# Kernel optimization log

Hardware: AMD Instinct MI355X
Metric: run time of the kernel (lower is better)

The kernel has to match this reference:

```python
import jax, jax.numpy as jnp
import numpy as np

N_NODES = 10000
N_EDGES = 160000
N_REL = 4
N_GRAPHS = 256
IN_DIM = 64


def rgcn_layer(x, W, root, bias, src, dst, etype, num_nodes, num_rel):
    # PyG RGCNConv with default aggr='mean': per-relation mean aggregation,
    # plus root transform and bias.
    h = jnp.einsum('nd,rdf->rnf', x, W)            # [R, N, F] grouped GEMM
    msg = h[etype, src]                             # [E, F] gather per edge
    comb = dst * num_rel + etype                    # (dst, relation) bucket
    cnt = jax.ops.segment_sum(jnp.ones(etype.shape, x.dtype), comb,
                              num_segments=num_nodes * num_rel)
    inv = 1.0 / jnp.maximum(cnt, 1.0)
    msg = msg * inv[comb][:, None]                  # per-relation mean norm
    agg = jax.ops.segment_sum(msg, dst, num_segments=num_nodes)  # scatter-add
    return agg + x @ root + bias


def global_mean_pool(x, batch, num_graphs):
    s = jax.ops.segment_sum(x, batch, num_segments=num_graphs)
    c = jax.ops.segment_sum(jnp.ones(batch.shape, x.dtype), batch,
                            num_segments=num_graphs)
    return s / jnp.maximum(c, 1.0)[:, None]


def setup_inputs() -> dict:
    key = jax.random.key(0)
    ks = jax.random.split(key, 20)
    s = 0.02
    inp = {
        'x': jax.random.normal(ks[0], (N_NODES, IN_DIM), jnp.float32),
        'edge_index': jax.random.randint(ks[1], (2, N_EDGES), 0, N_NODES),
        'edge_type': jax.random.randint(ks[2], (N_EDGES,), 0, N_REL),
        'batch': jnp.sort(jax.random.randint(ks[3], (N_NODES,), 0, N_GRAPHS)),
        'W1': jax.random.normal(ks[4], (N_REL, IN_DIM, 1024), jnp.float32) * s,
        'root1': jax.random.normal(ks[5], (IN_DIM, 1024), jnp.float32) * s,
        'b1': jnp.zeros((1024,), jnp.float32),
        'W2': jax.random.normal(ks[6], (N_REL, 1024, 1024), jnp.float32) * s,
        'root2': jax.random.normal(ks[7], (1024, 1024), jnp.float32) * s,
        'b2': jnp.zeros((1024,), jnp.float32),
        'W3': jax.random.normal(ks[8], (N_REL, 1024, 712), jnp.float32) * s,
        'root3': jax.random.normal(ks[9], (1024, 712), jnp.float32) * s,
        'b3': jnp.zeros((712,), jnp.float32),
        'fw1': jax.random.normal(ks[10], (712, 64), jnp.float32) * s,
        'fb1': jnp.zeros((64,), jnp.float32),
        'fw2': jax.random.normal(ks[11], (64, 1), jnp.float32) * s,
        'fb2': jnp.zeros((1,), jnp.float32),
    }
    return inp


def reference(x, edge_index, edge_type, batch, W1, root1, b1, W2, root2, b2,
              W3, root3, b3, fw1, fb1, fw2, fb2):
    src, dst = edge_index[0], edge_index[1]
    # dropout is a no-op in eval mode (training=False)
    h = jax.nn.relu(rgcn_layer(x, W1, root1, b1, src, dst, edge_type, N_NODES, N_REL))
    h = jax.nn.relu(rgcn_layer(h, W2, root2, b2, src, dst, edge_type, N_NODES, N_REL))
    h = jax.nn.relu(rgcn_layer(h, W3, root3, b3, src, dst, edge_type, N_NODES, N_REL))
    g = global_mean_pool(h, batch, N_GRAPHS)        # [G, 712]
    g = jax.nn.relu(g @ fw1 + fb1)
    out = g @ fw2 + fb2                             # [G, 1]
    return out
```

## Files before the change

### kernel.cpp

```cpp
#include <hip/hip_runtime.h>
#include <stdint.h>

#define N_NODES 10000
#define N_EDGES 160000
#define N_REL   4
#define N_GRAPHS 256
#define NBUCKET (N_NODES * N_REL)

typedef __attribute__((ext_vector_type(8))) short short8;
typedef __attribute__((ext_vector_type(4))) float float4v;

__device__ __forceinline__ unsigned short f2bf(float f) {
  unsigned int u = __float_as_uint(f);
  u = u + 0x7FFFu + ((u >> 16) & 1u);
  return (unsigned short)(u >> 16);
}
__device__ __forceinline__ float bf2f(unsigned short b) {
  return __uint_as_float(((unsigned int)b) << 16);
}

__device__ __forceinline__ void g2lds16(const void* g, void* l) {
  __builtin_amdgcn_global_load_lds(
      (const __attribute__((address_space(1))) void*)g,
      (__attribute__((address_space(3))) void*)l, 16, 0, 0);
}

__device__ __forceinline__ int lower_bound_i(const int* a, int n, int key) {
  int lo = 0, hi = n;
  while (lo < hi) { int mid = (lo + hi) >> 1; if (a[mid] < key) lo = mid + 1; else hi = mid; }
  return lo;
}

__global__ void count_edges_k(const int* __restrict__ ei, const int* __restrict__ et,
                              int* __restrict__ cnt, int E) {
  int e = blockIdx.x * 256 + threadIdx.x;
  if (e < E) atomicAdd(&cnt[ei[E + e] * N_REL + et[e]], 1);
}

__global__ void scan_block_k(const int* __restrict__ cnt, int* __restrict__ eexcl,
                             int* __restrict__ btot, int n) {
  int i = blockIdx.x * 256 + threadIdx.x;
  int v = (i < n) ? cnt[i] : 0;
  int lane = threadIdx.x & 63, wv = threadIdx.x >> 6;
  int s = v;
  #pragma unroll
  for (int off = 1; off < 64; off <<= 1) {
    int t = __shfl_up(s, off, 64);
    if (lane >= off) s += t;
  }
  __shared__ int wt[4];
  if (lane == 63) wt[wv] = s;
  __syncthreads();
  int wadd = 0;
  for (int w = 0; w < wv; ++w) wadd += wt[w];
  int incl = s + wadd;
  if (i < n) eexcl[i] = incl - v;
  if (threadIdx.x == 255) btot[blockIdx.x] = incl;
}

__global__ void scan_final_k(const int* __restrict__ cnt, const int* __restrict__ eexcl,
                             const int* __restrict__ btot, int* __restrict__ offs,
                             int* __restrict__ cursor, float* __restrict__ inv, int n) {
  __shared__ int wred[4];
  __shared__ int sboff;
  int t = threadIdx.x;
  int part = (t < (int)blockIdx.x) ? btot[t] : 0;
  #pragma unroll
  for (int off = 32; off > 0; off >>= 1) part += __shfl_down(part, off, 64);
  if ((t & 63) == 0) wred[t >> 6] = part;
  __syncthreads();
  if (t == 0) sboff = wred[0] + wred[1] + wred[2] + wred[3];
  __syncthreads();
  int i = blockIdx.x * 256 + t;
  if (i < n) {
    int o = sboff + eexcl[i];
    offs[i] = o;
    cursor[i] = o;
    int c = cnt[i];
    inv[i] = 1.0f / (float)(c > 1 ? c : 1);
  }
}

__global__ void fill_csr_k(const int* __restrict__ ei, const int* __restrict__ et,
                           int* __restrict__ cursor, int* __restrict__ elist, int E) {
  int e = blockIdx.x * 256 + threadIdx.x;
  if (e >= E) return;
  int dst = ei[E + e], src = ei[e], r = et[e];
  int pos = atomicAdd(&cursor[dst * N_REL + r], 1);
  elist[pos] = src;
}

__global__ void wcat_transpose_k(const float* __restrict__ W, const float* __restrict__ root,
                                 unsigned short* __restrict__ out, int Din4, int F, int K) {
  __shared__ float tile[32][33];
  int kb = blockIdx.x * 32, fb = blockIdx.y * 32;
  for (int i = threadIdx.y; i < 32; i += 8) {
    int k = kb + i, f = fb + threadIdx.x;
    float v = 0.0f;
    if (k < K && f < F) v = (k < Din4) ? W[(size_t)k * F + f] : root[(size_t)(k - Din4) * F + f];
    tile[i][threadIdx.x] = v;
  }
  __syncthreads();
  for (int i = threadIdx.y; i < 32; i += 8) {
    int f = fb + i, k = kb + threadIdx.x;
    if (f < F && k < K) out[(size_t)f * K + k] = f2bf(tile[threadIdx.x][i]);
  }
}

__global__ void aggregate64_k(const float* __restrict__ x, const int* __restrict__ offs,
                              const int* __restrict__ cnt, const float* __restrict__ inv,
                              const int* __restrict__ elist, unsigned short* __restrict__ Xcat) {
  const int n = blockIdx.x;
  const int wv = threadIdx.x >> 6;
  const int col = threadIdx.x & 63;
  const int b = n * N_REL + wv;
  const int start = offs[b], c = cnt[b];
  const float sc = inv[b];
  float acc = 0.0f;
  for (int j = 0; j < c; ++j) {
    int s = elist[start + j];
    acc += x[(size_t)s * 64 + col];
  }
  Xcat[(size_t)n * 320 + wv * 64 + col] = f2bf(acc * sc);
  if (wv == 0)
    Xcat[(size_t)n * 320 + 256 + col] = f2bf(x[(size_t)n * 64 + col]);
}

__global__ __launch_bounds__(64) void aggregate_bf16_k(
    const unsigned short* __restrict__ h,
    const int* __restrict__ offs, const int* __restrict__ cnt,
    const float* __restrict__ inv, const int* __restrict__ elist,
    unsigned short* __restrict__ Xcat) {
  const int bid = blockIdx.x;
  const int chunk = bid & 7;
  const int n = bid >> 3;
  const int lane = threadIdx.x;
  const int col = chunk * 128 + lane * 2;
  const int Din = 1024, K5 = 5120;
  const int b0 = n * N_REL;
  #pragma unroll
  for (int r = 0; r < N_REL; ++r) {
    const int s0 = offs[b0 + r];
    const int c = cnt[b0 + r];
    const float sc = inv[b0 + r];
    float a0 = 0.f, a1 = 0.f;
    for (int j = 0; j < c; ++j) {
      int s = elist[s0 + j];
      ushort2 v = *(const ushort2*)(h + (size_t)s * Din + col);
      a0 += bf2f(v.x); a1 += bf2f(v.y);
    }
    ushort2 o;
    o.x = f2bf(a0 * sc); o.y = f2bf(a1 * sc);
    *(ushort2*)&Xcat[(size_t)n * K5 + r * Din + col] = o;
  }
  *(ushort2*)&Xcat[(size_t)n * K5 + 4 * Din + col] =
      *(const ushort2*)(h + (size_t)n * Din + col);
}

__global__ __launch_bounds__(256) void gemm_bt_bias_relu_k(
    const short* __restrict__ A, const short* __restrict__ Bt,
    const float* __restrict__ bias, unsigned short* __restrict__ C,
    int M, int Ndim, int K, int NX) {
  __shared__ short As[128 * 64];
  __shared__ short Bs[128 * 64];

  const int bid = blockIdx.x;
  const int xcd = bid & 7;
  const int local = bid >> 3;
  const int t = xcd * (NX * 10) + local;
  const int tileM = t / NX;
  const int tileN = t - tileM * NX;
  const int mBase = tileM * 128;
  const int nBase = tileN * 128;

  const int tid = threadIdx.x;
  const int wave = tid >> 6;
  const int lane = tid & 63;
  const int half = lane >> 4;
  const int lrow = lane & 15;
  const int wm = (wave >> 1) * 64;
  const int wn = (wave & 1) * 64;
  const int srow = lane >> 3;
  const int schunk = (lane & 7) ^ srow;

  float4v acc[4][4] = {};

  for (int k0 = 0; k0 < K; k0 += 64) {
    #pragma unroll
    for (int p = 0; p < 4; ++p) {
      int rb = wave * 32 + p * 8;
      int r = rb + srow;
      int gr = mBase + r; if (gr > M - 1) gr = M - 1;
      g2lds16(A + (size_t)gr * K + k0 + schunk * 8, &As[rb * 64]);
      int gn = nBase + r; if (gn > Ndim - 1) gn = Ndim - 1;
      g2lds16(Bt + (size_t)gn * K + k0 + schunk * 8, &Bs[rb * 64]);
    }
    __syncthreads();

    #pragma unroll
    for (int kk = 0; kk < 2; ++kk) {
      short8 a[4], b[4];
      #pragma unroll
      for (int i = 0; i < 4; ++i) {
        int r = wm + i * 16 + lrow;
        int q = (kk * 4 + half) ^ (r & 7);
        a[i] = *(const short8*)&As[r * 64 + q * 8];
      }
      #pragma unroll
      for (int j = 0; j < 4; ++j) {
        int r = wn + j * 16 + lrow;
        int q = (kk * 4 + half) ^ (r & 7);
        b[j] = *(const short8*)&Bs[r * 64 + q * 8];
      }
      #pragma unroll
      for (int i = 0; i < 4; ++i)
        #pragma unroll
        for (int j = 0; j < 4; ++j)
          acc[i][j] = __builtin_amdgcn_mfma_f32_16x16x32_bf16(a[i], b[j], acc[i][j], 0, 0, 0);
    }
    __syncthreads();
  }

  #pragma unroll
  for (int i = 0; i < 4; ++i) {
    int row0 = mBase + wm + i * 16 + half * 4;
    #pragma unroll
    for (int j = 0; j < 4; ++j) {
      int col = nBase + wn + j * 16 + lrow;
      if (col < Ndim) {
        float bv = bias[col];
        #pragma unroll
        for (int r = 0; r < 4; ++r) {
          int rr = row0 + r;
          if (rr < M) C[(size_t)rr * Ndim + col] = f2bf(fmaxf(acc[i][j][r] + bv, 0.0f));
        }
      }
    }
  }
}

__global__ __launch_bounds__(256) void pool_mlp_k(
    const unsigned short* __restrict__ h, const int* __restrict__ batch,
    const float* __restrict__ fw1, const float* __restrict__ fb1,
    const float* __restrict__ fw2, const float* __restrict__ fb2,
    float* __restrict__ out, int N, int F) {
  __shared__ float gsh[712];
  __shared__ float part[4][64];

  const int gid = blockIdx.x;
  const int tid = threadIdx.x;
  const int lo = lower_bound_i(batch, N, gid);
  const int hi = lower_bound_i(batch, N, gid + 1);
  const float scale = (hi > lo) ? 1.0f / (float)(hi - lo) : 0.0f;
  const int C4 = F >> 2;

  if (tid < C4) {
    float a0 = 0.f, a1 = 0.f, a2 = 0.f, a3 = 0.f;
    for (int n = lo; n < hi; ++n) {
      ushort4 v = *(const ushort4*)(h + (size_t)n * F + tid * 4);
      a0 += bf2f(v.x); a1 += bf2f(v.y); a2 += bf2f(v.z); a3 += bf2f(v.w);
    }
    gsh[tid * 4 + 0] = a0 * scale;
    gsh[tid * 4 + 1] = a1 * scale;
    gsh[tid * 4 + 2] = a2 * scale;
    gsh[tid * 4 + 3] = a3 * scale;
  }
  __syncthreads();

  const int f = tid & 63;
  const int wv = tid >> 6;
  const int d0 = wv * 178;
  const int d1 = min(d0 + 178, F);
  float a = 0.0f;
  int d = d0;
  for (; d + 3 < d1; d += 4) {
    float g0 = gsh[d], g1 = gsh[d + 1], g2 = gsh[d + 2], g3 = gsh[d + 3];
    a += g0 * fw1[(size_t)d * 64 + f]
       + g1 * fw1[(size_t)(d + 1) * 64 + f]
       + g2 * fw1[(size_t)(d + 2) * 64 + f]
       + g3 * fw1[(size_t)(d + 3) * 64 + f];
  }
  for (; d < d1; ++d) a += gsh[d] * fw1[(size_t)d * 64 + f];
  part[wv][f] = a;
  __syncthreads();

  if (tid < 64) {
    float hsum = part[0][tid] + part[1][tid] + part[2][tid] + part[3][tid] + fb1[tid];
    hsum = fmaxf(hsum, 0.0f);
    float p = hsum * fw2[tid];
    #pragma unroll
    for (int off = 32; off > 0; off >>= 1) p += __shfl_down(p, off, 64);
    if (tid == 0) out[gid] = p + fb2[0];
  }
}

extern "C" void kernel_launch(void* const* d_in, const int* in_sizes, int n_in,
                              void* d_out, int out_size, void* d_ws, size_t ws_size,
                              hipStream_t stream) {
  (void)in_sizes; (void)n_in; (void)out_size;
  const float* x    = (const float*)d_in[0];
  const int*  ei    = (const int*)d_in[1];
  const int*  et    = (const int*)d_in[2];
  const int*  batch = (const int*)d_in[3];
  const float* W1 = (const float*)d_in[4],  *root1 = (const float*)d_in[5],  *b1 = (const float*)d_in[6];
  const float* W2 = (const float*)d_in[7],  *root2 = (const float*)d_in[8],  *b2 = (const float*)d_in[9];
  const float* W3 = (const float*)d_in[10], *root3 = (const float*)d_in[11], *b3 = (const float*)d_in[12];
  const float* fw1 = (const float*)d_in[13], *fb1 = (const float*)d_in[14];
  const float* fw2 = (const float*)d_in[15], *fb2 = (const float*)d_in[16];
  float* out = (float*)d_out;

  char* ws = (char*)d_ws;
  size_t off = 0;
  auto alloc = [&](size_t bytes) -> void* {
    void* p = ws + off; off += (bytes + 255) & ~(size_t)255; return p;
  };
  int*   cnt    = (int*)alloc(NBUCKET * 4);
  int*   offs   = (int*)alloc(NBUCKET * 4);
  int*   cursor = (int*)alloc(NBUCKET * 4);
  int*   eexcl  = (int*)alloc(NBUCKET * 4);
  int*   btot   = (int*)alloc(256 * 4);
  int*   elist  = (int*)alloc(N_EDGES * 4);
  float* inv    = (float*)alloc(NBUCKET * 4);
  unsigned short* Xcat  = (unsigned short*)alloc((size_t)N_NODES * 5120 * 2);
  unsigned short* WcatT = (unsigned short*)alloc((size_t)1024 * 5120 * 2);
  unsigned short* hA = (unsigned short*)alloc((size_t)N_NODES * 1024 * 2);
  unsigned short* hB = (unsigned short*)alloc((size_t)N_NODES * 1024 * 2);
  (void)ws_size;

  hipMemsetAsync(cnt, 0, NBUCKET * 4, stream);
  count_edges_k<<<(N_EDGES + 255) / 256, 256, 0, stream>>>(ei, et, cnt, N_EDGES);
  int nsb = (NBUCKET + 255) / 256;
  scan_block_k<<<nsb, 256, 0, stream>>>(cnt, eexcl, btot, NBUCKET);
  scan_final_k<<<nsb, 256, 0, stream>>>(cnt, eexcl, btot, offs, cursor, inv, NBUCKET);
  fill_csr_k<<<(N_EDGES + 255) / 256, 256, 0, stream>>>(ei, et, cursor, elist, N_EDGES);

  wcat_transpose_k<<<dim3(10, 32), dim3(32, 8), 0, stream>>>(W1, root1, WcatT, 256, 1024, 320);
  aggregate64_k<<<N_NODES, 256, 0, stream>>>(x, offs, cnt, inv, elist, Xcat);
  gemm_bt_bias_relu_k<<<8 * 80, 256, 0, stream>>>(
      (const short*)Xcat, (const short*)WcatT, b1, hA, N_NODES, 1024, 320, 8);

  wcat_transpose_k<<<dim3(160, 32), dim3(32, 8), 0, stream>>>(W2, root2, WcatT, 4096, 1024, 5120);
  aggregate_bf16_k<<<N_NODES * 8, 64, 0, stream>>>(hA, offs, cnt, inv, elist, Xcat);
  gemm_bt_bias_relu_k<<<8 * 80, 256, 0, stream>>>(
      (const short*)Xcat, (const short*)WcatT, b2, hB, N_NODES, 1024, 5120, 8);

  wcat_transpose_k<<<dim3(160, 23), dim3(32, 8), 0, stream>>>(W3, root3, WcatT, 4096, 712, 5120);
  aggregate_bf16_k<<<N_NODES * 8, 64, 0, stream>>>(hB, offs, cnt, inv, elist, Xcat);
  gemm_bt_bias_relu_k<<<6 * 80, 256, 0, stream>>>(
      (const short*)Xcat, (const short*)WcatT, b3, hA, N_NODES, 712, 5120, 6);

  pool_mlp_k<<<N_GRAPHS, 256, 0, stream>>>(hA, batch, fw1, fb1, fw2, fb2, out,
                                           N_NODES, 712);
}
```

Baseline: 596.7 us.

## Parallelize relation buckets across waves and batch edge-index loads in aggregation

The bf16 aggregation kernel now uses 256-thread blocks, so each of four waves handles one relation bucket at the same time instead of looping over relations serially. Edge indices are loaded cooperatively, 64 at a time per wave, and broadcast with shuffles. The gather loop is unrolled by four to keep more independent loads in flight. Outputs are written with nontemporal stores to avoid polluting the cache, at the cost of idle waves when relation bucket sizes are uneven.

Result: slower. 667.9 us (+11.9%).

```diff
diff --git a/kernel.cpp b/kernel.cpp
--- a/kernel.cpp
+++ b/kernel.cpp
@@ -126,7 +126,7 @@
     Xcat[(size_t)n * 320 + 256 + col] = f2bf(x[(size_t)n * 64 + col]);
 }
 
-__global__ __launch_bounds__(64) void aggregate_bf16_k(
+__global__ __launch_bounds__(256) void aggregate_bf16_k(
     const unsigned short* __restrict__ h,
     const int* __restrict__ offs, const int* __restrict__ cnt,
     const float* __restrict__ inv, const int* __restrict__ elist,
@@ -134,27 +134,45 @@
   const int bid = blockIdx.x;
   const int chunk = bid & 7;
   const int n = bid >> 3;
-  const int lane = threadIdx.x;
+  const int wv = threadIdx.x >> 6;
+  const int lane = threadIdx.x & 63;
   const int col = chunk * 128 + lane * 2;
   const int Din = 1024, K5 = 5120;
-  const int b0 = n * N_REL;
-  #pragma unroll
-  for (int r = 0; r < N_REL; ++r) {
-    const int s0 = offs[b0 + r];
-    const int c = cnt[b0 + r];
-    const float sc = inv[b0 + r];
-    float a0 = 0.f, a1 = 0.f;
-    for (int j = 0; j < c; ++j) {
-      int s = elist[s0 + j];
-      ushort2 v = *(const ushort2*)(h + (size_t)s * Din + col);
+  const int b = n * N_REL + wv;
+  const int s0 = offs[b];
+  const int c = cnt[b];
+  const float sc = inv[b];
+
+  float a0 = 0.f, a1 = 0.f;
+  for (int base = 0; base < c; base += 64) {
+    int m = min(64, c - base);
+    int eid = (lane < m) ? elist[s0 + base + lane] : 0;
+    int j = 0;
+    for (; j + 3 < m; j += 4) {
+      int e0 = __shfl(eid, j, 64),     e1 = __shfl(eid, j + 1, 64);
+      int e2 = __shfl(eid, j + 2, 64), e3 = __shfl(eid, j + 3, 64);
+      ushort2 v0 = *(const ushort2*)(h + (size_t)e0 * Din + col);
+      ushort2 v1 = *(const ushort2*)(h + (size_t)e1 * Din + col);
+      ushort2 v2 = *(const ushort2*)(h + (size_t)e2 * Din + col);
+      ushort2 v3 = *(const ushort2*)(h + (size_t)e3 * Din + col);
+      a0 += bf2f(v0.x); a1 += bf2f(v0.y);
+      a0 += bf2f(v1.x); a1 += bf2f(v1.y);
+      a0 += bf2f(v2.x); a1 += bf2f(v2.y);
+      a0 += bf2f(v3.x); a1 += bf2f(v3.y);
+    }
+    for (; j < m; ++j) {
+      int e = __shfl(eid, j, 64);
+      ushort2 v = *(const ushort2*)(h + (size_t)e * Din + col);
       a0 += bf2f(v.x); a1 += bf2f(v.y);
     }
-    ushort2 o;
-    o.x = f2bf(a0 * sc); o.y = f2bf(a1 * sc);
-    *(ushort2*)&Xcat[(size_t)n * K5 + r * Din + col] = o;
-  }
-  *(ushort2*)&Xcat[(size_t)n * K5 + 4 * Din + col] =
-      *(const ushort2*)(h + (size_t)n * Din + col);
+  }
+
+  unsigned int o = (unsigned int)f2bf(a0 * sc) | ((unsigned int)f2bf(a1 * sc) << 16);
+  __builtin_nontemporal_store(o, (unsigned int*)&Xcat[(size_t)n * K5 + wv * Din + col]);
+  if (wv == 0) {
+    unsigned int rv = *(const unsigned int*)(h + (size_t)n * Din + col);
+    __builtin_nontemporal_store(rv, (unsigned int*)&Xcat[(size_t)n * K5 + 4 * Din + col]);
+  }
 }
 
 __global__ __launch_bounds__(256) void gemm_bt_bias_relu_k(
@@ -340,12 +358,12 @@
       (const short*)Xcat, (const short*)WcatT, b1, hA, N_NODES, 1024, 320, 8);
 
   wcat_transpose_k<<<dim3(160, 32), dim3(32, 8), 0, stream>>>(W2, root2, WcatT, 4096, 1024, 5120);
-  aggregate_bf16_k<<<N_NODES * 8, 64, 0, stream>>>(hA, offs, cnt, inv, elist, Xcat);
+  aggregate_bf16_k<<<N_NODES * 8, 256, 0, stream>>>(hA, offs, cnt, inv, elist, Xcat);
   gemm_bt_bias_relu_k<<<8 * 80, 256, 0, stream>>>(
       (const short*)Xcat, (const short*)WcatT, b2, hB, N_NODES, 1024, 5120, 8);
 
   wcat_transpose_k<<<dim3(160, 23), dim3(32, 8), 0, stream>>>(W3, root3, WcatT, 4096, 712, 5120);
-  aggregate_bf16_k<<<N_NODES * 8, 64, 0, stream>>>(hB, offs, cnt, inv, elist, Xcat);
+  aggregate_bf16_k<<<N_NODES * 8, 256, 0, stream>>>(hB, offs, cnt, inv, elist, Xcat);
   gemm_bt_bias_relu_k<<<6 * 80, 256, 0, stream>>>(
       (const short*)Xcat, (const short*)WcatT, b3, hA, N_NODES, 712, 5120, 6);
 
```
